# Optimization experiments

Measured on AMD Instinct MI355X. Metric: run time of the kernel, lower is better.

Reference implementation:

```python
import jax, jax.numpy as jnp
import numpy as np

B, S, D, H = 8, 2048, 1024, 16
HD = D // H  # head_dim = 64


def setup_inputs() -> dict:
    key = jax.random.key(0)
    ks = jax.random.split(key, 10)
    s = 0.02
    return {
        "x": jax.random.normal(ks[0], (B, S, D), jnp.float32),
        "mask": jnp.zeros((B, 1, S), jnp.float32),
        "Wq": jax.random.normal(ks[1], (D, D), jnp.float32) * s,
        "bq": jnp.zeros((D,), jnp.float32),
        "Wk": jax.random.normal(ks[2], (D, D), jnp.float32) * s,
        "bk": jnp.zeros((D,), jnp.float32),
        "Wv": jax.random.normal(ks[3], (D, D), jnp.float32) * s,
        "bv": jnp.zeros((D,), jnp.float32),
        "wa": jax.random.normal(ks[4], (HD, 1), jnp.float32) * s,
        "ba": jnp.zeros((1,), jnp.float32),
        "wb": jax.random.normal(ks[5], (HD, 1), jnp.float32) * s,
        "bb": jnp.zeros((1,), jnp.float32),
        "Wu": jax.random.normal(ks[6], (HD, HD), jnp.float32) * s,
        "bu": jnp.zeros((HD,), jnp.float32),
        "Wo": jax.random.normal(ks[7], (D, D), jnp.float32) * s,
        "bo": jnp.zeros((D,), jnp.float32),
        "gamma": jnp.ones((D,), jnp.float32),
        "beta_ln": jnp.zeros((D,), jnp.float32),
    }


def _split_heads(t):
    # [B,S,D] -> [B,H,S,HD]
    return t.reshape(B, S, H, HD).transpose(0, 2, 1, 3)


def reference(x, mask, Wq, bq, Wk, bk, Wv, bv, wa, ba, wb, bb, Wu, bu, Wo, bo, gamma, beta_ln):
    scale = 1.0 / jnp.sqrt(jnp.float32(HD))
    q = _split_heads(x @ Wq + bq)  # [B,H,S,HD]
    k = _split_heads(x @ Wk + bk)
    v = _split_heads(x @ Wv + bv)

    # additive attention over queries -> global query vector per head
    alphascore = (jnp.squeeze(q @ wa, -1) + ba[0]) * scale + mask  # [B,H,S]
    alphaw = jax.nn.softmax(alphascore, axis=-1)
    q_av = jnp.einsum('bhs,bhsd->bhd', alphaw, q)

    p = k * q_av[:, :, None, :]  # gated keys [B,H,S,HD]
    betascore = (jnp.squeeze(p @ wb, -1) + bb[0]) * scale + mask
    betaw = jax.nn.softmax(betascore, axis=-1)
    p_av = jnp.einsum('bhs,bhsd->bhd', betaw, p)

    u = v * p_av[:, :, None, :]  # gated values
    r = u @ Wu + bu  # [B,H,S,HD]
    newr = (r + q).transpose(0, 2, 1, 3).reshape(B, S, D)
    attn_out = newr @ Wo + bo

    h = x + attn_out
    mu = jnp.mean(h, axis=-1, keepdims=True)
    var = jnp.mean(jnp.square(h - mu), axis=-1, keepdims=True)
    return (h - mu) * jax.lax.rsqrt(var + 1e-6) * gamma + beta_ln
```

## Files before the change

kernel.cpp:

```cpp
#include <hip/hip_runtime.h>
#include <cstdint>

#define BB 8
#define SS 2048
#define DD 1024
#define HH 16
#define HDIM 64
#define MTOT (BB*SS)
#define NQKV 3072

typedef __attribute__((ext_vector_type(8))) __bf16 bf16x8;
typedef __attribute__((ext_vector_type(4))) float f32x4;

#define AS1(p) ((const __attribute__((address_space(1))) void*)(p))
#define AS3(p) ((__attribute__((address_space(3))) void*)(p))

__device__ __forceinline__ float bf2f(uint16_t u){
  return __uint_as_float(((uint32_t)u) << 16);
}
__device__ __forceinline__ uint16_t f2bf(float f){
  uint32_t u = __float_as_uint(f);
  return (uint16_t)((u + 0x7fffu + ((u >> 16) & 1u)) >> 16);
}

__global__ __launch_bounds__(256)
void k_prep(const float* __restrict__ x,
            const float* __restrict__ Wq, const float* __restrict__ Wk,
            const float* __restrict__ Wv, const float* __restrict__ Wo,
            const float* __restrict__ bq, const float* __restrict__ bk,
            const float* __restrict__ bv,
            uint16_t* __restrict__ xb, uint16_t* __restrict__ Wt,
            uint16_t* __restrict__ WoT, float* __restrict__ bqkv)
{
  __shared__ float t[32][33];
  const int blk = blockIdx.x, tid = threadIdx.x;
  if (blk < 2048){
    const int n4 = MTOT*DD/4;
    for (int i = blk*256 + tid; i < n4; i += 2048*256){
      float4 v = reinterpret_cast<const float4*>(x)[i];
      ushort4 o;
      o.x = f2bf(v.x); o.y = f2bf(v.y); o.z = f2bf(v.z); o.w = f2bf(v.w);
      reinterpret_cast<ushort4*>(xb)[i] = o;
    }
  } else if (blk < 6144){
    const int zb = blk - 2048;
    const int z = zb >> 10, rem = zb & 1023;
    const int by = rem >> 5, bx = rem & 31;
    const float* src = (z==0)?Wq:(z==1)?Wk:(z==2)?Wv:Wo;
    uint16_t* dst = (z<3) ? (Wt + (size_t)z*1024*1024) : WoT;
    const int k0 = by*32, n0 = bx*32;
    const int tx = tid & 31, ty = tid >> 5;
    #pragma unroll
    for (int r = 0; r < 4; ++r)
      t[ty + r*8][tx] = src[(size_t)(k0 + ty + r*8)*1024 + n0 + tx];
    __syncthreads();
    #pragma unroll
    for (int r = 0; r < 4; ++r)
      dst[(size_t)(n0 + ty + r*8)*1024 + k0 + tx] = f2bf(t[tx][ty + r*8]);
  } else {
    const int i = (blk - 6144)*256 + tid;
    if (i < NQKV)
      bqkv[i] = (i < 1024) ? bq[i] : (i < 2048) ? bk[i-1024] : bv[i-2048];
  }
}


#define BARRIER __builtin_amdgcn_s_barrier()
#define LGKM0 { asm volatile("s_waitcnt lgkmcnt(0)" ::: "memory"); __builtin_amdgcn_sched_barrier(0); }

#define READA(BUF, MH) { \
  const uint16_t* _sl = lds + ((BUF)*4 + (MH))*8192; \
  _Pragma("unroll") \
  for (int f = 0; f < 4; ++f) \
    _Pragma("unroll") \
    for (int ks = 0; ks < 2; ++ks) \
      a[f][ks] = *(const bf16x8*)(_sl + (wm*64 + f*16 + l15)*64 + (((ks*4 + l4) ^ l7)<<3)); \
}

#define READB(BUF, NH, BV) { \
  const uint16_t* _sl = lds + ((BUF)*4 + 2 + (NH))*8192; \
  _Pragma("unroll") \
  for (int j = 0; j < 2; ++j) \
    _Pragma("unroll") \
    for (int ks = 0; ks < 2; ++ks) \
      BV[j][ks] = *(const bf16x8*)(_sl + (wn*32 + j*16 + l15)*64 + (((ks*4 + l4) ^ l7)<<3)); \
}

#define MMA(MH, NH, BV) { \
  __builtin_amdgcn_s_setprio(1); \
  _Pragma("unroll") \
  for (int ks = 0; ks < 2; ++ks) \
    _Pragma("unroll") \
    for (int f = 0; f < 4; ++f) \
      _Pragma("unroll") \
      for (int j = 0; j < 2; ++j) \
        acc[(MH)*4+f][(NH)*2+j] = __builtin_amdgcn_mfma_f32_16x16x32_bf16(a[f][ks], BV[j][ks], acc[(MH)*4+f][(NH)*2+j], 0, 0, 0); \
  __builtin_amdgcn_s_setprio(0); }

#define STAGEA(T, H) { \
  char* _d = (char*)lds + ((((T)&1)*4 + (H))*16384) + wave*1024; \
  _Pragma("unroll") \
  for (int l = 0; l < 2; ++l) \
    __builtin_amdgcn_global_load_lds(AS1(pA + (l*131072 + (H)*65536 + (T)*64)), AS3(_d + l*8192), 16, 0, 0); \
}

#define STAGEB(T, H) { \
  char* _d = (char*)lds + ((((T)&1)*4 + 2 + (H))*16384) + wave*1024; \
  _Pragma("unroll") \
  for (int l = 0; l < 2; ++l) \
    __builtin_amdgcn_global_load_lds(AS1(pB + (l*131072 + (H)*32768 + (T)*64)), AS3(_d + l*8192), 16, 0, 0); \
}

template<int EPI, int NB_T>
__global__ __launch_bounds__(512)
void k_gemm256(const uint16_t* __restrict__ A, const uint16_t* __restrict__ Bt,
               const float* __restrict__ bias, const uint16_t* __restrict__ resid16,
               uint16_t* __restrict__ Cout)
{
  constexpr int N = NB_T * 256;
  __shared__ uint16_t lds[8 * 8192];
  const int tid = threadIdx.x;
  const int lane = tid & 63, wave = tid >> 6;
  const int wm = wave >> 2, wn = wave & 3;
  const int l15 = lane & 15, l4 = lane >> 4, l7 = lane & 7;

  const int nwg = gridDim.x, cpx = nwg >> 3, bid = blockIdx.x;
  const int wg = (bid & 7) * cpx + (bid >> 3);
  const int m0 = (wg / NB_T) << 8, n0 = (wg % NB_T) << 8;

  const int colbase = (((tid & 7) ^ ((tid >> 3) & 7)) << 3);
  const uint16_t* pA = A  + (size_t)(m0 + (tid >> 3)) * 1024 + colbase;
  const uint16_t* pB = Bt + (size_t)(n0 + ((tid >> 8) << 6) + ((tid >> 3) & 31)) * 1024 + colbase;

  f32x4 acc[8][4] = {};
  bf16x8 a[4][2], b0[2][2], b1[2][2];

  STAGEA(0,0); STAGEB(0,1); STAGEA(0,1); STAGEB(0,0);
  STAGEA(1,0); STAGEB(1,1); STAGEA(1,1);
  asm volatile("s_waitcnt vmcnt(6)" ::: "memory");
  BARRIER;

  #pragma unroll
  for (int I = 0; I < 7; ++I){
    const int e = 2*I;
    READA(0,0); READB(0,0,b0); STAGEB(e+1, 0);
    BARRIER; LGKM0; MMA(0,0,b0); BARRIER;
    READB(0,1,b1); STAGEA(e+2, 0);
    BARRIER; LGKM0; MMA(0,1,b1); BARRIER;
    READA(0,1); STAGEB(e+2, 1);
    BARRIER; LGKM0; MMA(1,1,b1); BARRIER;
    STAGEA(e+2, 1);
    asm volatile("s_waitcnt vmcnt(6)" ::: "memory");
    BARRIER; LGKM0; MMA(1,0,b0); BARRIER;
    READA(1,0); READB(1,0,b0); STAGEB(e+2, 0);
    BARRIER; LGKM0; MMA(0,0,b0); BARRIER;
    READB(1,1,b1); STAGEA(e+3, 0);
    BARRIER; LGKM0; MMA(0,1,b1); BARRIER;
    READA(1,1); STAGEB(e+3, 1);
    BARRIER; LGKM0; MMA(1,1,b1); BARRIER;
    STAGEA(e+3, 1);
    asm volatile("s_waitcnt vmcnt(6)" ::: "memory");
    BARRIER; LGKM0; MMA(1,0,b0); BARRIER;
  }

  {
    READA(0,0); READB(0,0,b0); STAGEB(15, 0);
    BARRIER; LGKM0; MMA(0,0,b0); BARRIER;
    READB(0,1,b1);
    BARRIER; LGKM0; MMA(0,1,b1); BARRIER;
    READA(0,1);
    BARRIER; LGKM0; MMA(1,1,b1); BARRIER;
    asm volatile("s_waitcnt vmcnt(0)" ::: "memory");
    BARRIER; LGKM0; MMA(1,0,b0); BARRIER;
    READA(1,0); READB(1,0,b0);
    BARRIER; LGKM0; MMA(0,0,b0); BARRIER;
    READB(1,1,b1);
    BARRIER; LGKM0; MMA(0,1,b1); BARRIER;
    READA(1,1);
    BARRIER; LGKM0; MMA(1,1,b1); BARRIER;
    LGKM0; MMA(1,0,b0);
  }

  #pragma unroll
  for (int mh = 0; mh < 2; ++mh)
  #pragma unroll
  for (int f = 0; f < 4; ++f)
  #pragma unroll
  for (int nh = 0; nh < 2; ++nh)
  #pragma unroll
  for (int j = 0; j < 2; ++j){
    const int gcol = n0 + wn*64 + nh*32 + j*16 + l15;
    const float bi = bias[gcol];
    const int rbase = m0 + wm*128 + mh*64 + f*16 + l4*4;
    #pragma unroll
    for (int rr = 0; rr < 4; ++rr){
      const size_t idx = (size_t)(rbase + rr)*N + gcol;
      float v = acc[mh*4+f][nh*2+j][rr] + bi;
      if (EPI == 1) v += bf2f(resid16[idx]);
      Cout[idx] = f2bf(v);
    }
  }
}

__device__ __forceinline__ float block_red_max512(float v, float* red, int tid){
  red[tid] = v; __syncthreads();
  for (int off = 256; off > 0; off >>= 1){
    if (tid < off) red[tid] = fmaxf(red[tid], red[tid+off]);
    __syncthreads();
  }
  float r = red[0]; __syncthreads();
  return r;
}
__device__ __forceinline__ float block_red_sum512(float v, float* red, int tid){
  red[tid] = v; __syncthreads();
  for (int off = 256; off > 0; off >>= 1){
    if (tid < off) red[tid] += red[tid+off];
    __syncthreads();
  }
  float r = red[0]; __syncthreads();
  return r;
}

__device__ __forceinline__ void score_pass(const uint16_t* __restrict__ base,
    float biasv, const float* wv, float* sc, const float* __restrict__ mrow, int tid){
  for (int s = tid; s < SS; s += 512){
    const uint16_t* row = base + (size_t)s*NQKV;
    float acc = 0.f;
    #pragma unroll
    for (int jj = 0; jj < 8; ++jj){
      int4 raw = *(const int4*)(row + jj*8);
      unsigned uu[4] = {(unsigned)raw.x,(unsigned)raw.y,(unsigned)raw.z,(unsigned)raw.w};
      #pragma unroll
      for (int e = 0; e < 4; ++e){
        acc += __uint_as_float(uu[e] << 16)        * wv[jj*8 + 2*e]
             + __uint_as_float(uu[e] & 0xffff0000u) * wv[jj*8 + 2*e + 1];
      }
    }
    sc[s] = (acc + biasv)*0.125f + mrow[s];
  }
}

__device__ __forceinline__ void col_accum(const uint16_t* __restrict__ base,
    const float* sc, float part[8][64], int tid){
  const int j = tid & 63, g = tid >> 6;
  const uint16_t* p = base + (size_t)(g*256)*NQKV + j;
  float a = 0.f;
  for (int s = 0; s < 256; ++s)
    a += sc[g*256 + s] * bf2f(p[(size_t)s*NQKV]);
  part[g][j] = a;
}

__global__ __launch_bounds__(512)
void k_head(const uint16_t* __restrict__ qkv, const float* __restrict__ mask,
            const float* __restrict__ wa, const float* __restrict__ ba,
            const float* __restrict__ wb, const float* __restrict__ bbp,
            const float* __restrict__ Wu, uint16_t* __restrict__ WuPT)
{
  __shared__ float sc[SS];
  __shared__ float red[512];
  __shared__ float part[8][64];
  __shared__ float qav[64];
  __shared__ float wvec[64];
  __shared__ float pav[64];

  const int bh = blockIdx.x, b = bh >> 4, h = bh & 15;
  const int tid = threadIdx.x;
  const uint16_t* qb  = qkv + (size_t)b*SS*NQKV + h*64;
  const uint16_t* kb2 = qb + 1024;
  const float* mrow = mask + b*SS;

  if (tid < 64) wvec[tid] = wa[tid];
  __syncthreads();

  score_pass(qb, ba[0], wvec, sc, mrow, tid);
  __syncthreads();
  float lm = -3.4e38f;
  for (int s = tid; s < SS; s += 512) lm = fmaxf(lm, sc[s]);
  float mx = block_red_max512(lm, red, tid);
  float ls = 0.f;
  for (int s = tid; s < SS; s += 512){ float e = __expf(sc[s]-mx); sc[s] = e; ls += e; }
  __syncthreads();
  float inv = 1.f / block_red_sum512(ls, red, tid);

  col_accum(qb, sc, part, tid);
  __syncthreads();
  if (tid < 64){
    float q = 0.f;
    #pragma unroll
    for (int g = 0; g < 8; ++g) q += part[g][tid];
    qav[tid] = q*inv;
    wvec[tid] = q*inv*wb[tid];
  }
  __syncthreads();

  score_pass(kb2, bbp[0], wvec, sc, mrow, tid);
  __syncthreads();
  lm = -3.4e38f;
  for (int s = tid; s < SS; s += 512) lm = fmaxf(lm, sc[s]);
  mx = block_red_max512(lm, red, tid);
  ls = 0.f;
  for (int s = tid; s < SS; s += 512){ float e = __expf(sc[s]-mx); sc[s] = e; ls += e; }
  __syncthreads();
  float inv2 = 1.f / block_red_sum512(ls, red, tid);

  col_accum(kb2, sc, part, tid);
  __syncthreads();
  if (tid < 64){
    float p = 0.f;
    #pragma unroll
    for (int g = 0; g < 8; ++g) p += part[g][tid];
    pav[tid] = qav[tid]*p*inv2;
  }
  __syncthreads();

  uint16_t* dst = WuPT + (size_t)bh*4096;
  for (int idx = tid; idx < 4096; idx += 512){
    const int i = idx & 63, jcol = idx >> 6;
    dst[idx] = f2bf(pav[i]*Wu[i*64 + jcol]);
  }
}

__global__ __launch_bounds__(256)
void k_newr(const uint16_t* __restrict__ qkv, const uint16_t* __restrict__ WuPT,
            const float* __restrict__ bu, uint16_t* __restrict__ newr)
{
  const int bh = blockIdx.x >> 3, st = blockIdx.x & 7;
  const int b = bh >> 4, h = bh & 15;
  const int tid = threadIdx.x, wave = tid >> 6, lane = tid & 63;
  const int l15 = lane & 15, l4 = lane >> 4;
  const int s0 = st*256 + wave*64;
  const uint16_t* vb = qkv + 2048 + h*64;
  const uint16_t* wt = WuPT + (size_t)bh*4096;

  f32x4 acc[4][4] = {};
  #pragma unroll
  for (int ks = 0; ks < 2; ++ks){
    bf16x8 bfr[4];
    #pragma unroll
    for (int n = 0; n < 4; ++n)
      bfr[n] = *(const bf16x8*)(wt + (n*16 + l15)*64 + ks*32 + l4*8);
    #pragma unroll
    for (int m = 0; m < 4; ++m){
      const int s = s0 + m*16 + l15;
      bf16x8 af = *(const bf16x8*)(vb + (size_t)(b*SS + s)*NQKV + ks*32 + l4*8);
      #pragma unroll
      for (int n = 0; n < 4; ++n)
        acc[m][n] = __builtin_amdgcn_mfma_f32_16x16x32_bf16(af, bfr[n], acc[m][n], 0, 0, 0);
    }
  }
  #pragma unroll
  for (int n = 0; n < 4; ++n){
    const int j = n*16 + l15;
    const float bj = bu[j];
    #pragma unroll
    for (int m = 0; m < 4; ++m){
      #pragma unroll
      for (int r = 0; r < 4; ++r){
        const int s = s0 + m*16 + l4*4 + r;
        const size_t qidx = (size_t)(b*SS + s)*NQKV + h*64 + j;
        const float q = bf2f(qkv[qidx]);
        newr[(size_t)(b*SS + s)*DD + h*64 + j] = f2bf(acc[m][n][r] + bj + q);
      }
    }
  }
}

__global__ __launch_bounds__(256)
void k_ln(const uint16_t* __restrict__ h16, const float* __restrict__ gamma,
          const float* __restrict__ beta, float* __restrict__ out)
{
  __shared__ float r1[256], r2[256];
  const int row = blockIdx.x, tid = threadIdx.x;
  const ushort4 hv = ((const ushort4*)(h16 + (size_t)row*DD))[tid];
  float v0 = bf2f(hv.x), v1 = bf2f(hv.y), v2 = bf2f(hv.z), v3 = bf2f(hv.w);
  float s  = v0 + v1 + v2 + v3;
  float ss = v0*v0 + v1*v1 + v2*v2 + v3*v3;
  r1[tid] = s; r2[tid] = ss; __syncthreads();
  for (int off = 128; off > 0; off >>= 1){
    if (tid < off){ r1[tid] += r1[tid+off]; r2[tid] += r2[tid+off]; }
    __syncthreads();
  }
  const float mu  = r1[0]*(1.f/1024.f);
  const float var = r2[0]*(1.f/1024.f) - mu*mu;
  const float inv = rsqrtf(var + 1e-6f);
  const float4 g  = ((const float4*)gamma)[tid];
  const float4 be = ((const float4*)beta)[tid];
  float4 o;
  o.x = (v0-mu)*inv*g.x + be.x;
  o.y = (v1-mu)*inv*g.y + be.y;
  o.z = (v2-mu)*inv*g.z + be.z;
  o.w = (v3-mu)*inv*g.w + be.w;
  ((float4*)(out + (size_t)row*DD))[tid] = o;
}

extern "C" void kernel_launch(void* const* d_in, const int* in_sizes, int n_in,
                              void* d_out, int out_size, void* d_ws, size_t ws_size,
                              hipStream_t stream) {
  const float* x    = (const float*)d_in[0];
  const float* mask = (const float*)d_in[1];
  const float* Wq   = (const float*)d_in[2];
  const float* bq   = (const float*)d_in[3];
  const float* Wk   = (const float*)d_in[4];
  const float* bk   = (const float*)d_in[5];
  const float* Wv   = (const float*)d_in[6];
  const float* bv   = (const float*)d_in[7];
  const float* wa   = (const float*)d_in[8];
  const float* ba   = (const float*)d_in[9];
  const float* wb   = (const float*)d_in[10];
  const float* bb   = (const float*)d_in[11];
  const float* Wu   = (const float*)d_in[12];
  const float* bu   = (const float*)d_in[13];
  const float* Wo   = (const float*)d_in[14];
  const float* bo   = (const float*)d_in[15];
  const float* gamma= (const float*)d_in[16];
  const float* beta = (const float*)d_in[17];
  float* out = (float*)d_out;

  char* ws = (char*)d_ws;
  const size_t MB = 1ull << 20;
  uint16_t* xb    = (uint16_t*)(ws);
  uint16_t* Wt    = (uint16_t*)(ws + 32*MB);
  uint16_t* WoT   = (uint16_t*)(ws + 38*MB);
  float*    bqkv  = (float*)   (ws + 40*MB);
  uint16_t* WuPT  = (uint16_t*)(ws + 41*MB);
  uint16_t* qkv   = (uint16_t*)(ws + 42*MB);
  uint16_t* newr  = (uint16_t*)(ws + 138*MB);
  uint16_t* hbuf16= (uint16_t*)(ws + 42*MB);

  k_prep<<<6156, 256, 0, stream>>>(x, Wq, Wk, Wv, Wo, bq, bk, bv, xb, Wt, WoT, bqkv);

  k_gemm256<0,12><<<(MTOT/256)*(NQKV/256), 512, 0, stream>>>(xb, Wt, bqkv, nullptr, qkv);
  k_head<<<BB*HH, 512, 0, stream>>>(qkv, mask, wa, ba, wb, bb, Wu, WuPT);
  k_newr<<<BB*HH*8, 256, 0, stream>>>(qkv, WuPT, bu, newr);
  k_gemm256<1,4><<<(MTOT/256)*(DD/256), 512, 0, stream>>>(newr, WoT, bo, xb, hbuf16);
  k_ln<<<MTOT, 256, 0, stream>>>(hbuf16, gamma, beta, out);
}
```

Baseline: 254.9 us.

## Double-buffer GEMM fragment registers to overlap LDS reads with MFMA

The GEMM main loop switches to ping-pong register fragments (aP/aQ, bP/bQ), so LDS reads for the next MFMA block are issued while the current block runs. The explicit lgkmcnt(0) waits and about half of the barriers are removed, and the vmcnt wait threshold changes. This is meant to hide LDS latency and cut sync stalls, in exchange for more VGPR pressure. It also leaves the compiler to place the LDS waits, which may weaken ordering against global_load_lds writes.

```diff
diff --git a/kernel.cpp b/kernel.cpp
--- a/kernel.cpp
+++ b/kernel.cpp
@@ -66,27 +66,28 @@
 
 
 #define BARRIER __builtin_amdgcn_s_barrier()
-#define LGKM0 { asm volatile("s_waitcnt lgkmcnt(0)" ::: "memory"); __builtin_amdgcn_sched_barrier(0); }
-
-#define READA(BUF, MH) { \
+#define VMCNT4  asm volatile("s_waitcnt vmcnt(4)" ::: "memory")
+#define VMCNT0  asm volatile("s_waitcnt vmcnt(0)" ::: "memory")
+
+#define READA_(BUF, MH, DST) { \
   const uint16_t* _sl = lds + ((BUF)*4 + (MH))*8192; \
   _Pragma("unroll") \
   for (int f = 0; f < 4; ++f) \
     _Pragma("unroll") \
     for (int ks = 0; ks < 2; ++ks) \
-      a[f][ks] = *(const bf16x8*)(_sl + (wm*64 + f*16 + l15)*64 + (((ks*4 + l4) ^ l7)<<3)); \
-}
-
-#define READB(BUF, NH, BV) { \
+      DST[f][ks] = *(const bf16x8*)(_sl + (wm*64 + f*16 + l15)*64 + (((ks*4 + l4) ^ l7)<<3)); \
+}
+
+#define READB_(BUF, NH, DST) { \
   const uint16_t* _sl = lds + ((BUF)*4 + 2 + (NH))*8192; \
   _Pragma("unroll") \
   for (int j = 0; j < 2; ++j) \
     _Pragma("unroll") \
     for (int ks = 0; ks < 2; ++ks) \
-      BV[j][ks] = *(const bf16x8*)(_sl + (wn*32 + j*16 + l15)*64 + (((ks*4 + l4) ^ l7)<<3)); \
-}
-
-#define MMA(MH, NH, BV) { \
+      DST[j][ks] = *(const bf16x8*)(_sl + (wn*32 + j*16 + l15)*64 + (((ks*4 + l4) ^ l7)<<3)); \
+}
+
+#define MMA_(MH, NH, AV, BV) { \
   __builtin_amdgcn_s_setprio(1); \
   _Pragma("unroll") \
   for (int ks = 0; ks < 2; ++ks) \
@@ -94,7 +95,7 @@
     for (int f = 0; f < 4; ++f) \
       _Pragma("unroll") \
       for (int j = 0; j < 2; ++j) \
-        acc[(MH)*4+f][(NH)*2+j] = __builtin_amdgcn_mfma_f32_16x16x32_bf16(a[f][ks], BV[j][ks], acc[(MH)*4+f][(NH)*2+j], 0, 0, 0); \
+        acc[(MH)*4+f][(NH)*2+j] = __builtin_amdgcn_mfma_f32_16x16x32_bf16(AV[f][ks], BV[j][ks], acc[(MH)*4+f][(NH)*2+j], 0, 0, 0); \
   __builtin_amdgcn_s_setprio(0); }
 
 #define STAGEA(T, H) { \
@@ -133,52 +134,41 @@
   const uint16_t* pB = Bt + (size_t)(n0 + ((tid >> 8) << 6) + ((tid >> 3) & 31)) * 1024 + colbase;
 
   f32x4 acc[8][4] = {};
-  bf16x8 a[4][2], b0[2][2], b1[2][2];
+  bf16x8 aP[4][2], aQ[4][2];
+  bf16x8 bP[2][2], bQ[2][2];
 
   STAGEA(0,0); STAGEB(0,1); STAGEA(0,1); STAGEB(0,0);
-  STAGEA(1,0); STAGEB(1,1); STAGEA(1,1);
-  asm volatile("s_waitcnt vmcnt(6)" ::: "memory");
+  STAGEA(1,0); STAGEB(1,1);
+  VMCNT4;
+  STAGEA(1,1);
   BARRIER;
+  READA_(0,0,aP); READB_(0,0,bP);
 
   #pragma unroll
   for (int I = 0; I < 7; ++I){
     const int e = 2*I;
-    READA(0,0); READB(0,0,b0); STAGEB(e+1, 0);
-    BARRIER; LGKM0; MMA(0,0,b0); BARRIER;
-    READB(0,1,b1); STAGEA(e+2, 0);
-    BARRIER; LGKM0; MMA(0,1,b1); BARRIER;
-    READA(0,1); STAGEB(e+2, 1);
-    BARRIER; LGKM0; MMA(1,1,b1); BARRIER;
-    STAGEA(e+2, 1);
-    asm volatile("s_waitcnt vmcnt(6)" ::: "memory");
-    BARRIER; LGKM0; MMA(1,0,b0); BARRIER;
-    READA(1,0); READB(1,0,b0); STAGEB(e+2, 0);
-    BARRIER; LGKM0; MMA(0,0,b0); BARRIER;
-    READB(1,1,b1); STAGEA(e+3, 0);
-    BARRIER; LGKM0; MMA(0,1,b1); BARRIER;
-    READA(1,1); STAGEB(e+3, 1);
-    BARRIER; LGKM0; MMA(1,1,b1); BARRIER;
-    STAGEA(e+3, 1);
-    asm volatile("s_waitcnt vmcnt(6)" ::: "memory");
-    BARRIER; LGKM0; MMA(1,0,b0); BARRIER;
+    READB_(0,1,bQ); STAGEB(e+1,0); MMA_(0,0,aP,bP); BARRIER;
+    READA_(0,1,aQ); STAGEA(e+2,0); MMA_(0,1,aP,bQ); BARRIER;
+    STAGEB(e+2,1); MMA_(1,1,aQ,bQ); BARRIER;
+    VMCNT4; BARRIER;
+    READA_(1,0,aP); READB_(1,0,bQ); STAGEA(e+2,1); MMA_(1,0,aQ,bP); BARRIER;
+    READB_(1,1,bP); STAGEB(e+2,0); MMA_(0,0,aP,bQ); BARRIER;
+    READA_(1,1,aQ); STAGEA(e+3,0); MMA_(0,1,aP,bP); BARRIER;
+    STAGEB(e+3,1); MMA_(1,1,aQ,bP); BARRIER;
+    VMCNT4; BARRIER;
+    READA_(0,0,aP); READB_(0,0,bP); STAGEA(e+3,1); MMA_(1,0,aQ,bQ); BARRIER;
   }
 
   {
-    READA(0,0); READB(0,0,b0); STAGEB(15, 0);
-    BARRIER; LGKM0; MMA(0,0,b0); BARRIER;
-    READB(0,1,b1);
-    BARRIER; LGKM0; MMA(0,1,b1); BARRIER;
-    READA(0,1);
-    BARRIER; LGKM0; MMA(1,1,b1); BARRIER;
-    asm volatile("s_waitcnt vmcnt(0)" ::: "memory");
-    BARRIER; LGKM0; MMA(1,0,b0); BARRIER;
-    READA(1,0); READB(1,0,b0);
-    BARRIER; LGKM0; MMA(0,0,b0); BARRIER;
-    READB(1,1,b1);
-    BARRIER; LGKM0; MMA(0,1,b1); BARRIER;
-    READA(1,1);
-    BARRIER; LGKM0; MMA(1,1,b1); BARRIER;
-    LGKM0; MMA(1,0,b0);
+    READB_(0,1,bQ); STAGEB(15,0); MMA_(0,0,aP,bP); BARRIER;
+    READA_(0,1,aQ); MMA_(0,1,aP,bQ); BARRIER;
+    MMA_(1,1,aQ,bQ); BARRIER;
+    VMCNT0; BARRIER;
+    READA_(1,0,aP); READB_(1,0,bQ); MMA_(1,0,aQ,bP); BARRIER;
+    READB_(1,1,bP); MMA_(0,0,aP,bQ); BARRIER;
+    READA_(1,1,aQ); MMA_(0,1,aP,bP); BARRIER;
+    MMA_(1,1,aQ,bP); BARRIER;
+    MMA_(1,0,aQ,bQ);
   }
 
   #pragma unroll
```

New measurement: 281.0 us. 10.2% more time.

## Stage head slices into LDS with online softmax; drop explicit LDS waits in GEMM

Applied to the files above, without the earlier changes.

The per-head pooling kernel now copies each 1024-row chunk of the Q or K head slice into LDS with global_load_lds. It then computes the scores, the softmax and the weighted column sums from LDS, merging the two chunks with an online max/sum rescale. Before, it read the strided global data twice per pass, once for scores and once for column accumulation. Separately, the GEMM main loop drops the explicit lgkmcnt(0) waits and sched_barriers, leaving the compiler to place LDS waits and schedule around them. The pooling change uses about 128KB of LDS per block, which limits it to one block per CU.

```diff
diff --git a/kernel.cpp b/kernel.cpp
--- a/kernel.cpp
+++ b/kernel.cpp
@@ -66,7 +66,6 @@
 
 
 #define BARRIER __builtin_amdgcn_s_barrier()
-#define LGKM0 { asm volatile("s_waitcnt lgkmcnt(0)" ::: "memory"); __builtin_amdgcn_sched_barrier(0); }
 
 #define READA(BUF, MH) { \
   const uint16_t* _sl = lds + ((BUF)*4 + (MH))*8192; \
@@ -144,41 +143,41 @@
   for (int I = 0; I < 7; ++I){
     const int e = 2*I;
     READA(0,0); READB(0,0,b0); STAGEB(e+1, 0);
-    BARRIER; LGKM0; MMA(0,0,b0); BARRIER;
+    BARRIER; MMA(0,0,b0); BARRIER;
     READB(0,1,b1); STAGEA(e+2, 0);
-    BARRIER; LGKM0; MMA(0,1,b1); BARRIER;
+    BARRIER; MMA(0,1,b1); BARRIER;
     READA(0,1); STAGEB(e+2, 1);
-    BARRIER; LGKM0; MMA(1,1,b1); BARRIER;
+    BARRIER; MMA(1,1,b1); BARRIER;
     STAGEA(e+2, 1);
     asm volatile("s_waitcnt vmcnt(6)" ::: "memory");
-    BARRIER; LGKM0; MMA(1,0,b0); BARRIER;
+    BARRIER; MMA(1,0,b0); BARRIER;
     READA(1,0); READB(1,0,b0); STAGEB(e+2, 0);
-    BARRIER; LGKM0; MMA(0,0,b0); BARRIER;
+    BARRIER; MMA(0,0,b0); BARRIER;
     READB(1,1,b1); STAGEA(e+3, 0);
-    BARRIER; LGKM0; MMA(0,1,b1); BARRIER;
+    BARRIER; MMA(0,1,b1); BARRIER;
     READA(1,1); STAGEB(e+3, 1);
-    BARRIER; LGKM0; MMA(1,1,b1); BARRIER;
+    BARRIER; MMA(1,1,b1); BARRIER;
     STAGEA(e+3, 1);
     asm volatile("s_waitcnt vmcnt(6)" ::: "memory");
-    BARRIER; LGKM0; MMA(1,0,b0); BARRIER;
+    BARRIER; MMA(1,0,b0); BARRIER;
   }
 
   {
     READA(0,0); READB(0,0,b0); STAGEB(15, 0);
-    BARRIER; LGKM0; MMA(0,0,b0); BARRIER;
+    BARRIER; MMA(0,0,b0); BARRIER;
     READB(0,1,b1);
-    BARRIER; LGKM0; MMA(0,1,b1); BARRIER;
+    BARRIER; MMA(0,1,b1); BARRIER;
     READA(0,1);
-    BARRIER; LGKM0; MMA(1,1,b1); BARRIER;
+    BARRIER; MMA(1,1,b1); BARRIER;
     asm volatile("s_waitcnt vmcnt(0)" ::: "memory");
-    BARRIER; LGKM0; MMA(1,0,b0); BARRIER;
+    BARRIER; MMA(1,0,b0); BARRIER;
     READA(1,0); READB(1,0,b0);
-    BARRIER; LGKM0; MMA(0,0,b0); BARRIER;
+    BARRIER; MMA(0,0,b0); BARRIER;
     READB(1,1,b1);
-    BARRIER; LGKM0; MMA(0,1,b1); BARRIER;
+    BARRIER; MMA(0,1,b1); BARRIER;
     READA(1,1);
-    BARRIER; LGKM0; MMA(1,1,b1); BARRIER;
-    LGKM0; MMA(1,0,b0);
+    BARRIER; MMA(1,1,b1); BARRIER;
+    MMA(1,0,b0);
   }
 
   #pragma unroll
@@ -221,33 +220,70 @@
   return r;
 }
 
-__device__ __forceinline__ void score_pass(const uint16_t* __restrict__ base,
-    float biasv, const float* wv, float* sc, const float* __restrict__ mrow, int tid){
-  for (int s = tid; s < SS; s += 512){
-    const uint16_t* row = base + (size_t)s*NQKV;
-    float acc = 0.f;
-    #pragma unroll
-    for (int jj = 0; jj < 8; ++jj){
-      int4 raw = *(const int4*)(row + jj*8);
-      unsigned uu[4] = {(unsigned)raw.x,(unsigned)raw.y,(unsigned)raw.z,(unsigned)raw.w};
+__device__ __forceinline__ void pool_pass(
+    const uint16_t* __restrict__ base, const float* __restrict__ mrow,
+    const float* __restrict__ wv, float biasv,
+    uint16_t* qlds, float* sc, float* red, float (*part)[64],
+    float* ca, float* scal, int tid, int wave, int lane)
+{
+  if (tid < 64) ca[tid] = 0.f;
+  if (tid == 0){ scal[0] = -3.4e38f; scal[1] = 0.f; }
+  __syncthreads();
+  #pragma unroll
+  for (int c = 0; c < 2; ++c){
+    {
+      const int r8 = lane >> 3, sl = lane & 7;
       #pragma unroll
-      for (int e = 0; e < 4; ++e){
-        acc += __uint_as_float(uu[e] << 16)        * wv[jj*8 + 2*e]
-             + __uint_as_float(uu[e] & 0xffff0000u) * wv[jj*8 + 2*e + 1];
+      for (int it = 0; it < 16; ++it){
+        const int rowg = c*1024 + (wave*16 + it)*8 + r8;
+        const uint16_t* src = base + (size_t)rowg*NQKV + ((sl ^ r8) << 3);
+        __builtin_amdgcn_global_load_lds(AS1(src),
+            AS3((char*)qlds + (wave*16 + it)*1024), 16, 0, 0);
       }
     }
-    sc[s] = (acc + biasv)*0.125f + mrow[s];
-  }
-}
-
-__device__ __forceinline__ void col_accum(const uint16_t* __restrict__ base,
-    const float* sc, float part[8][64], int tid){
-  const int j = tid & 63, g = tid >> 6;
-  const uint16_t* p = base + (size_t)(g*256)*NQKV + j;
-  float a = 0.f;
-  for (int s = 0; s < 256; ++s)
-    a += sc[g*256 + s] * bf2f(p[(size_t)s*NQKV]);
-  part[g][j] = a;
+    asm volatile("s_waitcnt vmcnt(0)" ::: "memory");
+    __syncthreads();
+    #pragma unroll
+    for (int rr = 0; rr < 2; ++rr){
+      const int row = tid + rr*512;
+      float acc = 0.f;
+      #pragma unroll
+      for (int jj = 0; jj < 8; ++jj){
+        bf16x8 v = *(const bf16x8*)(qlds + row*64 + ((jj ^ (row & 7)) << 3));
+        #pragma unroll
+        for (int e = 0; e < 8; ++e) acc += (float)v[e] * wv[jj*8 + e];
+      }
+      sc[row] = (acc + biasv)*0.125f + mrow[c*1024 + row];
+    }
+    __syncthreads();
+    const float lm = fmaxf(sc[tid], sc[tid+512]);
+    const float mx = block_red_max512(lm, red, tid);
+    const float e0 = __expf(sc[tid] - mx), e1 = __expf(sc[tid+512] - mx);
+    sc[tid] = e0; sc[tid+512] = e1;
+    const float lc = block_red_sum512(e0 + e1, red, tid);
+    {
+      const int j = tid & 63, g = tid >> 6;
+      const int slot_sh = j >> 3, jin = j & 7;
+      float a = 0.f;
+      for (int s = 0; s < 128; ++s){
+        const int row = g*128 + s;
+        a += sc[row] * bf2f(qlds[row*64 + (((slot_sh) ^ (row & 7)) << 3) + jin]);
+      }
+      part[g][j] = a;
+    }
+    __syncthreads();
+    if (tid < 64){
+      float colc = 0.f;
+      #pragma unroll
+      for (int g2 = 0; g2 < 8; ++g2) colc += part[g2][tid];
+      const float m_old = scal[0], l_old = scal[1];
+      const float m_new = fmaxf(m_old, mx);
+      const float fo = __expf(m_old - m_new), fc = __expf(mx - m_new);
+      ca[tid] = ca[tid]*fo + colc*fc;
+      if (tid == 0){ scal[1] = l_old*fo + lc*fc; scal[0] = m_new; }
+    }
+    __syncthreads();
+  }
 }
 
 __global__ __launch_bounds__(512)
@@ -256,61 +292,33 @@
             const float* __restrict__ wb, const float* __restrict__ bbp,
             const float* __restrict__ Wu, uint16_t* __restrict__ WuPT)
 {
-  __shared__ float sc[SS];
+  __shared__ uint16_t qlds[1024*64];
+  __shared__ float sc[1024];
   __shared__ float red[512];
   __shared__ float part[8][64];
-  __shared__ float qav[64];
-  __shared__ float wvec[64];
-  __shared__ float pav[64];
+  __shared__ float ca[64];
+  __shared__ float qav[64], wvec[64], wva[64], pav[64];
+  __shared__ float scal[2];
 
   const int bh = blockIdx.x, b = bh >> 4, h = bh & 15;
-  const int tid = threadIdx.x;
+  const int tid = threadIdx.x, wave = tid >> 6, lane = tid & 63;
   const uint16_t* qb  = qkv + (size_t)b*SS*NQKV + h*64;
   const uint16_t* kb2 = qb + 1024;
   const float* mrow = mask + b*SS;
 
-  if (tid < 64) wvec[tid] = wa[tid];
+  if (tid < 64) wva[tid] = wa[tid];
   __syncthreads();
 
-  score_pass(qb, ba[0], wvec, sc, mrow, tid);
+  pool_pass(qb, mrow, wva, ba[0], qlds, sc, red, part, ca, scal, tid, wave, lane);
+  if (tid < 64){
+    const float qv = ca[tid] / scal[1];
+    qav[tid] = qv;
+    wvec[tid] = qv * wb[tid];
+  }
   __syncthreads();
-  float lm = -3.4e38f;
-  for (int s = tid; s < SS; s += 512) lm = fmaxf(lm, sc[s]);
-  float mx = block_red_max512(lm, red, tid);
-  float ls = 0.f;
-  for (int s = tid; s < SS; s += 512){ float e = __expf(sc[s]-mx); sc[s] = e; ls += e; }
-  __syncthreads();
-  float inv = 1.f / block_red_sum512(ls, red, tid);
-
-  col_accum(qb, sc, part, tid);
-  __syncthreads();
-  if (tid < 64){
-    float q = 0.f;
-    #pragma unroll
-    for (int g = 0; g < 8; ++g) q += part[g][tid];
-    qav[tid] = q*inv;
-    wvec[tid] = q*inv*wb[tid];
-  }
-  __syncthreads();
-
-  score_pass(kb2, bbp[0], wvec, sc, mrow, tid);
-  __syncthreads();
-  lm = -3.4e38f;
-  for (int s = tid; s < SS; s += 512) lm = fmaxf(lm, sc[s]);
-  mx = block_red_max512(lm, red, tid);
-  ls = 0.f;
-  for (int s = tid; s < SS; s += 512){ float e = __expf(sc[s]-mx); sc[s] = e; ls += e; }
-  __syncthreads();
-  float inv2 = 1.f / block_red_sum512(ls, red, tid);
-
-  col_accum(kb2, sc, part, tid);
-  __syncthreads();
-  if (tid < 64){
-    float p = 0.f;
-    #pragma unroll
-    for (int g = 0; g < 8; ++g) p += part[g][tid];
-    pav[tid] = qav[tid]*p*inv2;
-  }
+
+  pool_pass(kb2, mrow, wvec, bbp[0], qlds, sc, red, part, ca, scal, tid, wave, lane);
+  if (tid < 64) pav[tid] = qav[tid] * (ca[tid] / scal[1]);
   __syncthreads();
 
   uint16_t* dst = WuPT + (size_t)bh*4096;
```

After: 229.8 us. 9.8% less time.
